# Kernel optimization log

Hardware: AMD Instinct MI355X
Metric: run time of the kernel (lower is better)

The kernel has to match this reference:

```python
import jax, jax.numpy as jnp
import numpy as np

N_NODES = 50000
N_EDGES = 800000
IN_DIM = 64
HID = 128
OUT_DIM = 128
N_LAYERS = 3
LN_EPS = 1e-5


def setup_inputs() -> dict:
    key = jax.random.key(0)
    ks = jax.random.split(key, 12)
    x = jax.random.normal(ks[0], (N_NODES, IN_DIM), dtype=jnp.float32)
    edge_index = jax.random.randint(ks[1], (2, N_EDGES), 0, N_NODES, dtype=jnp.int32)
    # parameters
    W_in = jax.random.normal(ks[2], (IN_DIM, HID), dtype=jnp.float32) / np.sqrt(IN_DIM)
    b_in = jnp.zeros((HID,), dtype=jnp.float32)
    W_layers = jax.random.normal(ks[3], (N_LAYERS, HID, HID), dtype=jnp.float32) / np.sqrt(HID)
    b_layers = jnp.zeros((N_LAYERS, HID), dtype=jnp.float32)
    ln_g = jnp.ones((N_LAYERS, HID), dtype=jnp.float32)
    ln_b = jnp.zeros((N_LAYERS, HID), dtype=jnp.float32)
    W_out = jax.random.normal(ks[4], (HID, OUT_DIM), dtype=jnp.float32) / np.sqrt(HID)
    b_out = jnp.zeros((OUT_DIM,), dtype=jnp.float32)
    return {
        "x": x, "edge_index": edge_index, "num_nodes_actual": 48000,
        "W_in": W_in, "b_in": b_in,
        "W_layers": W_layers, "b_layers": b_layers,
        "ln_g": ln_g, "ln_b": ln_b,
        "W_out": W_out, "b_out": b_out,
    }


def _layer_norm(h, g, b):
    mu = jnp.mean(h, axis=-1, keepdims=True)
    var = jnp.mean(jnp.square(h - mu), axis=-1, keepdims=True)
    return (h - mu) * jax.lax.rsqrt(var + LN_EPS) * g + b


def reference(x, edge_index, num_nodes_actual, W_in, b_in, W_layers, b_layers, ln_g, ln_b, W_out, b_out):
    n = x.shape[0]
    src, dst = edge_index[0], edge_index[1]
    # degree-normalized scatter-add aggregation (same for all layers)
    degree = jax.ops.segment_sum(jnp.ones_like(src, dtype=x.dtype), dst, num_segments=n)
    inv_deg = 1.0 / jnp.clip(degree, 1.0)[:, None]  # [N,1]

    h = x @ W_in + b_in  # [N, HID]
    for i in range(N_LAYERS):
        residual = h
        agg = jax.ops.segment_sum(h[src], dst, num_segments=n) * inv_deg
        h = (h + agg) @ W_layers[i] + b_layers[i]
        h = _layer_norm(h, ln_g[i], ln_b[i])
        h = jax.nn.relu(h)
        h = h + residual
    h = h @ W_out + b_out  # [N, OUT_DIM]
    # mean over actual (non-padding) nodes, keepdim
    return jnp.mean(h[:num_nodes_actual], axis=0, keepdims=True)  # [1, OUT_DIM]
```

## Files before the change

### kernel.cpp

```cpp
#include <hip/hip_runtime.h>

#define HID 128
#define INP 64
#define LN_EPS 1e-5f
#define RT 64

typedef __attribute__((ext_vector_type(8))) short bf16x8;
typedef __attribute__((ext_vector_type(4))) float f32x4;

__device__ __forceinline__ unsigned f2bf(float f) {
    unsigned u = __float_as_uint(f);
    return (u + 0x7FFFu + ((u >> 16) & 1u)) >> 16;
}
__device__ __forceinline__ float bflo(unsigned v) { return __uint_as_float(v << 16); }
__device__ __forceinline__ float bfhi(unsigned v) { return __uint_as_float(v & 0xFFFF0000u); }

__global__ __launch_bounds__(256) void k_count(const int* __restrict__ dst, int nE, int* __restrict__ cnt,
                                               int* __restrict__ rank, int nEdgeThreads,
                                               const float* __restrict__ W_in, const float* __restrict__ W_l,
                                               unsigned short* __restrict__ Wt_in, unsigned short* __restrict__ Wt_l) {
    int t = blockIdx.x * 256 + threadIdx.x;
    if (t < nEdgeThreads) {
        int base = t * 16;
        if (base + 16 <= nE) {
            int4 d[4];
#pragma unroll
            for (int j = 0; j < 4; ++j) d[j] = *reinterpret_cast<const int4*>(dst + base + j * 4);
            int p[16];
#pragma unroll
            for (int j = 0; j < 4; ++j) {
                p[j * 4 + 0] = atomicAdd(&cnt[d[j].x], 1);
                p[j * 4 + 1] = atomicAdd(&cnt[d[j].y], 1);
                p[j * 4 + 2] = atomicAdd(&cnt[d[j].z], 1);
                p[j * 4 + 3] = atomicAdd(&cnt[d[j].w], 1);
            }
#pragma unroll
            for (int j = 0; j < 4; ++j)
                *reinterpret_cast<int4*>(rank + base + j * 4) =
                    make_int4(p[j * 4 + 0], p[j * 4 + 1], p[j * 4 + 2], p[j * 4 + 3]);
        } else {
            for (int e = base; e < nE; ++e) rank[e] = atomicAdd(&cnt[dst[e]], 1);
        }
        return;
    }
    int i = t - nEdgeThreads;
    if (i < 128 * 64) {
        int col = i >> 6, k = i & 63;
        Wt_in[i] = (unsigned short)f2bf(W_in[(size_t)k * HID + col]);
    } else if (i < 128 * 64 + 3 * 128 * 128) {
        int j = i - 128 * 64;
        int l = j >> 14, r = j & 16383;
        int col = r >> 7, k = r & 127;
        Wt_l[j] = (unsigned short)f2bf(W_l[(size_t)l * 16384 + (size_t)k * HID + col]);
    }
}

__global__ void k_scan1(const int* __restrict__ cnt, int n, int* __restrict__ rowp, int* __restrict__ bsum) {
    __shared__ int s[256];
    int i = blockIdx.x * 256 + threadIdx.x;
    int v = (i < n) ? cnt[i] : 0;
    s[threadIdx.x] = v;
    __syncthreads();
    for (int off = 1; off < 256; off <<= 1) {
        int t = (threadIdx.x >= off) ? s[threadIdx.x - off] : 0;
        __syncthreads();
        s[threadIdx.x] += t;
        __syncthreads();
    }
    if (i < n) rowp[i] = s[threadIdx.x] - v;
    if (threadIdx.x == 255) bsum[blockIdx.x] = s[255];
}

__global__ void k_scan2(int* __restrict__ bsum, int nb) {
    __shared__ int s[256];
    int v = (threadIdx.x < nb) ? bsum[threadIdx.x] : 0;
    s[threadIdx.x] = v;
    __syncthreads();
    for (int off = 1; off < 256; off <<= 1) {
        int t = (threadIdx.x >= off) ? s[threadIdx.x - off] : 0;
        __syncthreads();
        s[threadIdx.x] += t;
        __syncthreads();
    }
    if (threadIdx.x < nb) bsum[threadIdx.x] = s[threadIdx.x] - v;
}

__global__ void k_scan3(int* __restrict__ rowp, const int* __restrict__ bsum, const int* __restrict__ cnt,
                        int n, int nE, float* __restrict__ invd) {
    int i = blockIdx.x * 256 + threadIdx.x;
    if (i < n) {
        int rp = rowp[i] + bsum[blockIdx.x];
        rowp[i] = rp;
        int c = cnt[i];
        invd[i] = 1.0f / (float)(c > 1 ? c : 1);
    } else if (i == n) {
        rowp[n] = nE;
    }
}

__global__ __launch_bounds__(256) void k_fill(const int* __restrict__ src, const int* __restrict__ dst,
                                              const int* __restrict__ rank, const int* __restrict__ rowp,
                                              int nE, int* __restrict__ csrc) {
    int t = blockIdx.x * 256 + threadIdx.x;
    int base = t * 16;
    if (base + 16 <= nE) {
        int4 d[4], s[4], r[4];
#pragma unroll
        for (int j = 0; j < 4; ++j) {
            d[j] = *reinterpret_cast<const int4*>(dst + base + j * 4);
            s[j] = *reinterpret_cast<const int4*>(src + base + j * 4);
            r[j] = *reinterpret_cast<const int4*>(rank + base + j * 4);
        }
#pragma unroll
        for (int j = 0; j < 4; ++j) {
            __builtin_nontemporal_store(s[j].x, &csrc[rowp[d[j].x] + r[j].x]);
            __builtin_nontemporal_store(s[j].y, &csrc[rowp[d[j].y] + r[j].y]);
            __builtin_nontemporal_store(s[j].z, &csrc[rowp[d[j].z] + r[j].z]);
            __builtin_nontemporal_store(s[j].w, &csrc[rowp[d[j].w] + r[j].w]);
        }
    } else if (base < nE) {
        for (int e = base; e < nE; ++e)
            __builtin_nontemporal_store(src[e], &csrc[rowp[dst[e]] + rank[e]]);
    }
}

__global__ __launch_bounds__(256) void k_inproj(const float* __restrict__ x,
                                                const unsigned short* __restrict__ Wt,
                                                const float* __restrict__ b,
                                                unsigned* __restrict__ hout, int n) {
    __shared__ unsigned short xs[RT * INP];
    const int tid = threadIdx.x;
    const int row0 = blockIdx.x * RT;

#pragma unroll
    for (int j = 0; j < 2; ++j) {
        int fid = tid + j * 256;
        int r = fid >> 3, c = fid & 7;
        int grow = row0 + r;
        unsigned o[4] = {0, 0, 0, 0};
        if (grow < n) {
            float4 v0 = *reinterpret_cast<const float4*>(x + (size_t)grow * INP + c * 8);
            float4 v1 = *reinterpret_cast<const float4*>(x + (size_t)grow * INP + c * 8 + 4);
            o[0] = f2bf(v0.x) | (f2bf(v0.y) << 16);
            o[1] = f2bf(v0.z) | (f2bf(v0.w) << 16);
            o[2] = f2bf(v1.x) | (f2bf(v1.y) << 16);
            o[3] = f2bf(v1.z) | (f2bf(v1.w) << 16);
        }
        int sw = c ^ (r & 7);
        *reinterpret_cast<uint4*>(xs + r * INP + sw * 8) = make_uint4(o[0], o[1], o[2], o[3]);
    }
    __syncthreads();

    const int l = tid & 63;
    const int w = tid >> 6;
    const int l15 = l & 15, lg = l >> 4;
    const int xrow = w * 16 + l15;

    f32x4 acc[8];
#pragma unroll
    for (int t = 0; t < 8; ++t) acc[t] = (f32x4){0.f, 0.f, 0.f, 0.f};

#pragma unroll
    for (int kc = 0; kc < 2; ++kc) {
        int bc = (kc * 4 + lg) ^ (xrow & 7);
        bf16x8 bfrag = *reinterpret_cast<const bf16x8*>(xs + xrow * INP + bc * 8);
        const unsigned short* wp = Wt + (size_t)l15 * INP + kc * 32 + lg * 8;
        bf16x8 af[8];
#pragma unroll
        for (int t = 0; t < 8; ++t) af[t] = *reinterpret_cast<const bf16x8*>(wp + (size_t)t * 16 * INP);
#pragma unroll
        for (int t = 0; t < 8; ++t)
            acc[t] = __builtin_amdgcn_mfma_f32_16x16x32_bf16(af[t], bfrag, acc[t], 0, 0, 0);
    }

    int grow = row0 + xrow;
    if (grow < n) {
#pragma unroll
        for (int t = 0; t < 8; ++t) {
            int c0 = t * 16 + lg * 4;
            f32x4 bb = *reinterpret_cast<const f32x4*>(b + c0);
            f32x4 o = acc[t] + bb;
            uint2 p;
            p.x = f2bf(o.x) | (f2bf(o.y) << 16);
            p.y = f2bf(o.z) | (f2bf(o.w) << 16);
            *reinterpret_cast<uint2*>(hout + (size_t)grow * 64 + t * 8 + lg * 2) = p;
        }
    }
}

__global__ __launch_bounds__(256) void k_agg(const unsigned* __restrict__ hb, const int* __restrict__ rowp,
                                             const int* __restrict__ csrc, const float* __restrict__ invd,
                                             unsigned* __restrict__ aggx, int n) {
    int node = blockIdx.x * 4 + (threadIdx.x >> 6);
    if (node >= n) return;
    int lane = threadIdx.x & 63;
    int e0 = rowp[node], e1 = rowp[node + 1];
    int deg = e1 - e0;
    unsigned self = hb[(size_t)node * 64 + lane];
    float inv = invd[node];
    float ax = 0.f, ay = 0.f;

    for (int base = 0; base < deg; base += 64) {
        int m = deg - base;
        if (m > 64) m = 64;
        int myidx = (base + lane < deg) ? csrc[e0 + base + lane] : 0;
        int j = 0;
        for (; j + 8 <= m; j += 8) {
            int s0 = __shfl(myidx, j + 0);
            int s1 = __shfl(myidx, j + 1);
            int s2 = __shfl(myidx, j + 2);
            int s3 = __shfl(myidx, j + 3);
            int s4 = __shfl(myidx, j + 4);
            int s5 = __shfl(myidx, j + 5);
            int s6 = __shfl(myidx, j + 6);
            int s7 = __shfl(myidx, j + 7);
            unsigned v0 = hb[(size_t)s0 * 64 + lane];
            unsigned v1 = hb[(size_t)s1 * 64 + lane];
            unsigned v2 = hb[(size_t)s2 * 64 + lane];
            unsigned v3 = hb[(size_t)s3 * 64 + lane];
            unsigned v4 = hb[(size_t)s4 * 64 + lane];
            unsigned v5 = hb[(size_t)s5 * 64 + lane];
            unsigned v6 = hb[(size_t)s6 * 64 + lane];
            unsigned v7 = hb[(size_t)s7 * 64 + lane];
            ax += ((bflo(v0) + bflo(v1)) + (bflo(v2) + bflo(v3))) +
                  ((bflo(v4) + bflo(v5)) + (bflo(v6) + bflo(v7)));
            ay += ((bfhi(v0) + bfhi(v1)) + (bfhi(v2) + bfhi(v3))) +
                  ((bfhi(v4) + bfhi(v5)) + (bfhi(v6) + bfhi(v7)));
        }
        for (; j < m; ++j) {
            int s0 = __shfl(myidx, j);
            unsigned v = hb[(size_t)s0 * 64 + lane];
            ax += bflo(v);
            ay += bfhi(v);
        }
    }

    float xlo = bflo(self) + ax * inv;
    float xhi = bfhi(self) + ay * inv;
    unsigned o = f2bf(xlo) | (f2bf(xhi) << 16);
    int c = lane >> 2;
    int sw = c ^ (node & 7);
    aggx[(size_t)node * 64 + sw * 4 + (lane & 3)] = o;
}

__global__ __launch_bounds__(256) void k_layer(const unsigned* __restrict__ hin,
                                               unsigned* __restrict__ hout,
                                               const unsigned* __restrict__ aggx,
                                               const unsigned short* __restrict__ Wt,
                                               const float* __restrict__ bias, const float* __restrict__ g,
                                               const float* __restrict__ lnb, int n) {
    const int tid = threadIdx.x;
    const int row0 = blockIdx.x * RT;
    const int lane = tid & 63;
    const int w = tid >> 6;
    const int l15 = lane & 15, lg = lane >> 4;
    const int xrow = w * 16 + l15;
    const int grow = row0 + xrow;

    const unsigned short* xg = reinterpret_cast<const unsigned short*>(aggx) + (size_t)grow * HID;

    f32x4 acc[8];
#pragma unroll
    for (int t = 0; t < 8; ++t) acc[t] = (f32x4){0.f, 0.f, 0.f, 0.f};

#pragma unroll
    for (int kc = 0; kc < 4; ++kc) {
        int bc = (kc * 4 + lg) ^ (xrow & 7);
        bf16x8 bfrag = *reinterpret_cast<const bf16x8*>(xg + bc * 8);
        const unsigned short* wp = Wt + (size_t)l15 * HID + kc * 32 + lg * 8;
        bf16x8 af[8];
#pragma unroll
        for (int t = 0; t < 8; ++t) af[t] = *reinterpret_cast<const bf16x8*>(wp + (size_t)t * 16 * HID);
#pragma unroll
        for (int t = 0; t < 8; ++t)
            acc[t] = __builtin_amdgcn_mfma_f32_16x16x32_bf16(af[t], bfrag, acc[t], 0, 0, 0);
    }

    float s = 0.f, q = 0.f;
#pragma unroll
    for (int t = 0; t < 8; ++t) {
        int c0 = t * 16 + lg * 4;
        f32x4 bb = *reinterpret_cast<const f32x4*>(bias + c0);
        acc[t] = acc[t] + bb;
        s += acc[t].x + acc[t].y + acc[t].z + acc[t].w;
        q += acc[t].x * acc[t].x + acc[t].y * acc[t].y + acc[t].z * acc[t].z + acc[t].w * acc[t].w;
    }
    s += __shfl_xor(s, 16, 64);
    s += __shfl_xor(s, 32, 64);
    q += __shfl_xor(q, 16, 64);
    q += __shfl_xor(q, 32, 64);
    float mu = s * (1.0f / HID);
    float var = q * (1.0f / HID) - mu * mu;
    float rs = rsqrtf(var + LN_EPS);

    if (grow < n) {
#pragma unroll
        for (int t = 0; t < 8; ++t) {
            int c0 = t * 16 + lg * 4;
            uint2 rv = *reinterpret_cast<const uint2*>(hin + (size_t)grow * 64 + t * 8 + lg * 2);
            f32x4 gv = *reinterpret_cast<const f32x4*>(g + c0);
            f32x4 lb = *reinterpret_cast<const f32x4*>(lnb + c0);
            float o0 = fmaxf((acc[t].x - mu) * rs * gv.x + lb.x, 0.f) + bflo(rv.x);
            float o1 = fmaxf((acc[t].y - mu) * rs * gv.y + lb.y, 0.f) + bfhi(rv.x);
            float o2 = fmaxf((acc[t].z - mu) * rs * gv.z + lb.z, 0.f) + bflo(rv.y);
            float o3 = fmaxf((acc[t].w - mu) * rs * gv.w + lb.w, 0.f) + bfhi(rv.y);
            uint2 p;
            p.x = f2bf(o0) | (f2bf(o1) << 16);
            p.y = f2bf(o2) | (f2bf(o3) << 16);
            *reinterpret_cast<uint2*>(hout + (size_t)grow * 64 + t * 8 + lg * 2) = p;
        }
    }
}

__global__ __launch_bounds__(256) void k_rowsum(const unsigned* __restrict__ hb, const int* __restrict__ n_act_p,
                                                float* __restrict__ accum, int n) {
    __shared__ float sred[256 * 2];
    int na = *n_act_p;
    int row0 = blockIdx.x * 256;
    int c = threadIdx.x & 63;
    int sub = threadIdx.x >> 6;
    int rend = row0 + 256;
    if (rend > na) rend = na;
    float sx = 0.f, sy = 0.f;
    for (int r = row0 + sub; r < rend; r += 4) {
        unsigned v = hb[(size_t)r * 64 + c];
        sx += bflo(v);
        sy += bfhi(v);
    }
    sred[threadIdx.x * 2] = sx;
    sred[threadIdx.x * 2 + 1] = sy;
    __syncthreads();
    if (threadIdx.x < 64) {
        float tx = sred[threadIdx.x * 2] + sred[(threadIdx.x + 64) * 2] +
                   sred[(threadIdx.x + 128) * 2] + sred[(threadIdx.x + 192) * 2];
        float ty = sred[threadIdx.x * 2 + 1] + sred[(threadIdx.x + 64) * 2 + 1] +
                   sred[(threadIdx.x + 128) * 2 + 1] + sred[(threadIdx.x + 192) * 2 + 1];
        if (row0 < na) {
            atomicAdd(&accum[2 * threadIdx.x], tx);
            atomicAdd(&accum[2 * threadIdx.x + 1], ty);
        }
    }
}

__global__ void k_out(const float* __restrict__ accum, const int* __restrict__ n_act_p,
                      const float* __restrict__ W_out, const float* __restrict__ b_out,
                      float* __restrict__ out) {
    __shared__ float m[HID];
    int c = threadIdx.x;
    float na = (float)(*n_act_p);
    m[c] = accum[c] / na;
    __syncthreads();
    float s = b_out[c];
    for (int k = 0; k < HID; ++k) s += m[k] * W_out[k * HID + c];
    out[c] = s;
}

extern "C" void kernel_launch(void* const* d_in, const int* in_sizes, int n_in,
                              void* d_out, int out_size, void* d_ws, size_t ws_size,
                              hipStream_t stream) {
    const int n  = in_sizes[0] / INP;
    const int nE = in_sizes[1] / 2;
    const float* x    = (const float*)d_in[0];
    const int*   ei   = (const int*)d_in[1];
    const int*   src  = ei;
    const int*   dst  = ei + nE;
    const int*   nact = (const int*)d_in[2];
    const float* W_in = (const float*)d_in[3];
    const float* b_in = (const float*)d_in[4];
    const float* W_l  = (const float*)d_in[5];
    const float* b_l  = (const float*)d_in[6];
    const float* lng  = (const float*)d_in[7];
    const float* lnb  = (const float*)d_in[8];
    const float* W_o  = (const float*)d_in[9];
    const float* b_o  = (const float*)d_in[10];

    char* ws = (char*)d_ws;
    size_t off = 0;
    auto alloc = [&](size_t bytes) {
        void* p = ws + off;
        off = (off + bytes + 255) & ~((size_t)255);
        return p;
    };
    unsigned* hbA  = (unsigned*)alloc((size_t)n * 64 * 4);
    unsigned* hbB  = (unsigned*)alloc((size_t)n * 64 * 4);
    unsigned* aggx = (unsigned*)alloc((size_t)(n + RT) * 64 * 4);
    int*   cnt  = (int*)alloc((size_t)n * 4);
    int*   rowp = (int*)alloc((size_t)(n + 1) * 4);
    float* invd = (float*)alloc((size_t)n * 4);
    int*   csrc = (int*)alloc((size_t)nE * 4);
    int*   rank = (int*)alloc((size_t)nE * 4);
    int*   bsum = (int*)alloc(1024);
    float* accum = (float*)alloc(HID * 4);
    unsigned short* Wt_in = (unsigned short*)alloc(128 * 64 * 2);
    unsigned short* Wt_l  = (unsigned short*)alloc(3 * 128 * 128 * 2);

    hipMemsetAsync(cnt, 0, (size_t)n * 4, stream);
    hipMemsetAsync(accum, 0, HID * 4, stream);

    int nb = (n + 255) / 256;
    int nEdgeThreads = (nE + 15) / 16;
    int nPrep = 128 * 64 + 3 * 128 * 128;
    int cpgrid = (nEdgeThreads + nPrep + 255) / 256;
    k_count<<<cpgrid, 256, 0, stream>>>(dst, nE, cnt, rank, nEdgeThreads, W_in, W_l, Wt_in, Wt_l);
    k_scan1<<<nb, 256, 0, stream>>>(cnt, n, rowp, bsum);
    k_scan2<<<1, 256, 0, stream>>>(bsum, nb);
    k_scan3<<<nb, 256, 0, stream>>>(rowp, bsum, cnt, n, nE, invd);
    k_fill<<<(nEdgeThreads + 255) / 256, 256, 0, stream>>>(src, dst, rank, rowp, nE, csrc);

    int tgrid = (n + RT - 1) / RT;
    k_inproj<<<tgrid, 256, 0, stream>>>(x, Wt_in, b_in, hbA, n);

    const unsigned* hin = hbA;
    unsigned* hout = hbB;
    for (int l = 0; l < 3; ++l) {
        k_agg<<<(n + 3) / 4, 256, 0, stream>>>(hin, rowp, csrc, invd, aggx, n);
        k_layer<<<tgrid, 256, 0, stream>>>(hin, hout, aggx,
                                           Wt_l + (size_t)l * 128 * 128,
                                           b_l + l * HID, lng + l * HID, lnb + l * HID, n);
        const unsigned* t = hout;
        hout = (unsigned*)hin;
        hin = t;
    }
    k_rowsum<<<(n + 255) / 256, 256, 0, stream>>>(hin, nact, accum, n);
    k_out<<<1, HID, 0, stream>>>(accum, nact, W_o, b_o, (float*)d_out);
}
```

Measured before the change: 294.0 us.

## Fuse scan stages, fill with input projection, final layer with row-sum; vectorize aggregation

Merges the block-offset scan into the final scan pass by having each block redo the small prefix over block sums. The CSR fill now runs in the same launch as the input projection, and the last layer's LayerNorm/residual output is reduced directly into the column accumulator, so the final hidden state is never written or re-read. The aggregation kernel now gathers 16-byte uint4 chunks with four edges per wavefront step and finishes with a cross-lane reduction. It also merges the two memsets into one by placing the buffers next to each other. Together these cut launches and memory traffic, at the cost of redundant scan work per block and more register pressure in the gather.

New measurement: 267.2 us (median of 2 runs). -9.1%, faster.

```diff
diff --git a/kernel.cpp b/kernel.cpp
--- a/kernel.cpp
+++ b/kernel.cpp
@@ -71,8 +71,10 @@
     if (threadIdx.x == 255) bsum[blockIdx.x] = s[255];
 }
 
-__global__ void k_scan2(int* __restrict__ bsum, int nb) {
+__global__ void k_scan3(int* __restrict__ rowp, const int* __restrict__ bsum, const int* __restrict__ cnt,
+                        int n, int nE, float* __restrict__ invd, int nb) {
     __shared__ int s[256];
+    __shared__ int boff;
     int v = (threadIdx.x < nb) ? bsum[threadIdx.x] : 0;
     s[threadIdx.x] = v;
     __syncthreads();
@@ -82,15 +84,11 @@
         s[threadIdx.x] += t;
         __syncthreads();
     }
-    if (threadIdx.x < nb) bsum[threadIdx.x] = s[threadIdx.x] - v;
-}
-
-__global__ void k_scan3(int* __restrict__ rowp, const int* __restrict__ bsum, const int* __restrict__ cnt,
-                        int n, int nE, float* __restrict__ invd) {
+    if (threadIdx.x == blockIdx.x) boff = s[threadIdx.x] - v;
+    __syncthreads();
     int i = blockIdx.x * 256 + threadIdx.x;
     if (i < n) {
-        int rp = rowp[i] + bsum[blockIdx.x];
-        rowp[i] = rp;
+        rowp[i] += boff;
         int c = cnt[i];
         invd[i] = 1.0f / (float)(c > 1 ? c : 1);
     } else if (i == n) {
@@ -98,40 +96,40 @@
     }
 }
 
-__global__ __launch_bounds__(256) void k_fill(const int* __restrict__ src, const int* __restrict__ dst,
-                                              const int* __restrict__ rank, const int* __restrict__ rowp,
-                                              int nE, int* __restrict__ csrc) {
-    int t = blockIdx.x * 256 + threadIdx.x;
-    int base = t * 16;
-    if (base + 16 <= nE) {
-        int4 d[4], s[4], r[4];
-#pragma unroll
-        for (int j = 0; j < 4; ++j) {
-            d[j] = *reinterpret_cast<const int4*>(dst + base + j * 4);
-            s[j] = *reinterpret_cast<const int4*>(src + base + j * 4);
-            r[j] = *reinterpret_cast<const int4*>(rank + base + j * 4);
-        }
-#pragma unroll
-        for (int j = 0; j < 4; ++j) {
-            __builtin_nontemporal_store(s[j].x, &csrc[rowp[d[j].x] + r[j].x]);
-            __builtin_nontemporal_store(s[j].y, &csrc[rowp[d[j].y] + r[j].y]);
-            __builtin_nontemporal_store(s[j].z, &csrc[rowp[d[j].z] + r[j].z]);
-            __builtin_nontemporal_store(s[j].w, &csrc[rowp[d[j].w] + r[j].w]);
-        }
-    } else if (base < nE) {
-        for (int e = base; e < nE; ++e)
-            __builtin_nontemporal_store(src[e], &csrc[rowp[dst[e]] + rank[e]]);
-    }
-}
-
-__global__ __launch_bounds__(256) void k_inproj(const float* __restrict__ x,
-                                                const unsigned short* __restrict__ Wt,
-                                                const float* __restrict__ b,
-                                                unsigned* __restrict__ hout, int n) {
+__global__ __launch_bounds__(256) void k_fillproj(const float* __restrict__ x,
+                                                  const unsigned short* __restrict__ Wt,
+                                                  const float* __restrict__ b,
+                                                  unsigned* __restrict__ hout, int n, int tgrid,
+                                                  const int* __restrict__ src, const int* __restrict__ dst,
+                                                  const int* __restrict__ rank, const int* __restrict__ rowp,
+                                                  int nE, int* __restrict__ csrc) {
+    const int tid = threadIdx.x;
+    if (blockIdx.x >= tgrid) {
+        int t = (blockIdx.x - tgrid) * 256 + tid;
+        int base = t * 16;
+        if (base + 16 <= nE) {
+            int4 d[4], s[4], r[4];
+#pragma unroll
+            for (int j = 0; j < 4; ++j) {
+                d[j] = *reinterpret_cast<const int4*>(dst + base + j * 4);
+                s[j] = *reinterpret_cast<const int4*>(src + base + j * 4);
+                r[j] = *reinterpret_cast<const int4*>(rank + base + j * 4);
+            }
+#pragma unroll
+            for (int j = 0; j < 4; ++j) {
+                __builtin_nontemporal_store(s[j].x, &csrc[rowp[d[j].x] + r[j].x]);
+                __builtin_nontemporal_store(s[j].y, &csrc[rowp[d[j].y] + r[j].y]);
+                __builtin_nontemporal_store(s[j].z, &csrc[rowp[d[j].z] + r[j].z]);
+                __builtin_nontemporal_store(s[j].w, &csrc[rowp[d[j].w] + r[j].w]);
+            }
+        } else if (base < nE) {
+            for (int e = base; e < nE; ++e)
+                __builtin_nontemporal_store(src[e], &csrc[rowp[dst[e]] + rank[e]]);
+        }
+        return;
+    }
     __shared__ unsigned short xs[RT * INP];
-    const int tid = threadIdx.x;
     const int row0 = blockIdx.x * RT;
-
 #pragma unroll
     for (int j = 0; j < 2; ++j) {
         int fid = tid + j * 256;
@@ -194,53 +192,65 @@
     int node = blockIdx.x * 4 + (threadIdx.x >> 6);
     if (node >= n) return;
     int lane = threadIdx.x & 63;
+    int grp = lane >> 4, cidx = lane & 15;
     int e0 = rowp[node], e1 = rowp[node + 1];
     int deg = e1 - e0;
-    unsigned self = hb[(size_t)node * 64 + lane];
-    float inv = invd[node];
-    float ax = 0.f, ay = 0.f;
+    const uint4* hb4 = reinterpret_cast<const uint4*>(hb);
+    float a0 = 0, a1 = 0, a2 = 0, a3 = 0, a4 = 0, a5 = 0, a6 = 0, a7 = 0;
 
     for (int base = 0; base < deg; base += 64) {
         int m = deg - base;
         if (m > 64) m = 64;
         int myidx = (base + lane < deg) ? csrc[e0 + base + lane] : 0;
-        int j = 0;
-        for (; j + 8 <= m; j += 8) {
-            int s0 = __shfl(myidx, j + 0);
-            int s1 = __shfl(myidx, j + 1);
-            int s2 = __shfl(myidx, j + 2);
-            int s3 = __shfl(myidx, j + 3);
-            int s4 = __shfl(myidx, j + 4);
-            int s5 = __shfl(myidx, j + 5);
-            int s6 = __shfl(myidx, j + 6);
-            int s7 = __shfl(myidx, j + 7);
-            unsigned v0 = hb[(size_t)s0 * 64 + lane];
-            unsigned v1 = hb[(size_t)s1 * 64 + lane];
-            unsigned v2 = hb[(size_t)s2 * 64 + lane];
-            unsigned v3 = hb[(size_t)s3 * 64 + lane];
-            unsigned v4 = hb[(size_t)s4 * 64 + lane];
-            unsigned v5 = hb[(size_t)s5 * 64 + lane];
-            unsigned v6 = hb[(size_t)s6 * 64 + lane];
-            unsigned v7 = hb[(size_t)s7 * 64 + lane];
-            ax += ((bflo(v0) + bflo(v1)) + (bflo(v2) + bflo(v3))) +
-                  ((bflo(v4) + bflo(v5)) + (bflo(v6) + bflo(v7)));
-            ay += ((bfhi(v0) + bfhi(v1)) + (bfhi(v2) + bfhi(v3))) +
-                  ((bfhi(v4) + bfhi(v5)) + (bfhi(v6) + bfhi(v7)));
-        }
-        for (; j < m; ++j) {
-            int s0 = __shfl(myidx, j);
-            unsigned v = hb[(size_t)s0 * 64 + lane];
-            ax += bflo(v);
-            ay += bfhi(v);
-        }
-    }
-
-    float xlo = bflo(self) + ax * inv;
-    float xhi = bfhi(self) + ay * inv;
-    unsigned o = f2bf(xlo) | (f2bf(xhi) << 16);
-    int c = lane >> 2;
-    int sw = c ^ (node & 7);
-    aggx[(size_t)node * 64 + sw * 4 + (lane & 3)] = o;
+        int steps = (m + 3) >> 2;
+        int jj = 0;
+        for (; jj + 4 <= steps; jj += 4) {
+            uint4 v[4];
+#pragma unroll
+            for (int k = 0; k < 4; ++k) {
+                int ei = (jj + k) * 4 + grp;
+                int s = __shfl(myidx, ei);
+                v[k] = (ei < m) ? hb4[(size_t)s * 16 + cidx] : make_uint4(0, 0, 0, 0);
+            }
+#pragma unroll
+            for (int k = 0; k < 4; ++k) {
+                a0 += bflo(v[k].x); a1 += bfhi(v[k].x);
+                a2 += bflo(v[k].y); a3 += bfhi(v[k].y);
+                a4 += bflo(v[k].z); a5 += bfhi(v[k].z);
+                a6 += bflo(v[k].w); a7 += bfhi(v[k].w);
+            }
+        }
+        for (; jj < steps; ++jj) {
+            int ei = jj * 4 + grp;
+            int s = __shfl(myidx, ei);
+            if (ei < m) {
+                uint4 v = hb4[(size_t)s * 16 + cidx];
+                a0 += bflo(v.x); a1 += bfhi(v.x);
+                a2 += bflo(v.y); a3 += bfhi(v.y);
+                a4 += bflo(v.z); a5 += bfhi(v.z);
+                a6 += bflo(v.w); a7 += bfhi(v.w);
+            }
+        }
+    }
+    a0 += __shfl_xor(a0, 16, 64); a0 += __shfl_xor(a0, 32, 64);
+    a1 += __shfl_xor(a1, 16, 64); a1 += __shfl_xor(a1, 32, 64);
+    a2 += __shfl_xor(a2, 16, 64); a2 += __shfl_xor(a2, 32, 64);
+    a3 += __shfl_xor(a3, 16, 64); a3 += __shfl_xor(a3, 32, 64);
+    a4 += __shfl_xor(a4, 16, 64); a4 += __shfl_xor(a4, 32, 64);
+    a5 += __shfl_xor(a5, 16, 64); a5 += __shfl_xor(a5, 32, 64);
+    a6 += __shfl_xor(a6, 16, 64); a6 += __shfl_xor(a6, 32, 64);
+    a7 += __shfl_xor(a7, 16, 64); a7 += __shfl_xor(a7, 32, 64);
+
+    if (grp == 0) {
+        float inv = invd[node];
+        uint4 self = hb4[(size_t)node * 16 + cidx];
+        unsigned o0 = f2bf(bflo(self.x) + a0 * inv) | (f2bf(bfhi(self.x) + a1 * inv) << 16);
+        unsigned o1 = f2bf(bflo(self.y) + a2 * inv) | (f2bf(bfhi(self.y) + a3 * inv) << 16);
+        unsigned o2 = f2bf(bflo(self.z) + a4 * inv) | (f2bf(bfhi(self.z) + a5 * inv) << 16);
+        unsigned o3 = f2bf(bflo(self.w) + a6 * inv) | (f2bf(bfhi(self.w) + a7 * inv) << 16);
+        int sw = cidx ^ (node & 7);
+        *reinterpret_cast<uint4*>(aggx + (size_t)node * 64 + sw * 4) = make_uint4(o0, o1, o2, o3);
+    }
 }
 
 __global__ __launch_bounds__(256) void k_layer(const unsigned* __restrict__ hin,
@@ -312,33 +322,90 @@
     }
 }
 
-__global__ __launch_bounds__(256) void k_rowsum(const unsigned* __restrict__ hb, const int* __restrict__ n_act_p,
-                                                float* __restrict__ accum, int n) {
-    __shared__ float sred[256 * 2];
-    int na = *n_act_p;
-    int row0 = blockIdx.x * 256;
-    int c = threadIdx.x & 63;
-    int sub = threadIdx.x >> 6;
-    int rend = row0 + 256;
-    if (rend > na) rend = na;
-    float sx = 0.f, sy = 0.f;
-    for (int r = row0 + sub; r < rend; r += 4) {
-        unsigned v = hb[(size_t)r * 64 + c];
-        sx += bflo(v);
-        sy += bfhi(v);
-    }
-    sred[threadIdx.x * 2] = sx;
-    sred[threadIdx.x * 2 + 1] = sy;
-    __syncthreads();
-    if (threadIdx.x < 64) {
-        float tx = sred[threadIdx.x * 2] + sred[(threadIdx.x + 64) * 2] +
-                   sred[(threadIdx.x + 128) * 2] + sred[(threadIdx.x + 192) * 2];
-        float ty = sred[threadIdx.x * 2 + 1] + sred[(threadIdx.x + 64) * 2 + 1] +
-                   sred[(threadIdx.x + 128) * 2 + 1] + sred[(threadIdx.x + 192) * 2 + 1];
-        if (row0 < na) {
-            atomicAdd(&accum[2 * threadIdx.x], tx);
-            atomicAdd(&accum[2 * threadIdx.x + 1], ty);
-        }
+__global__ __launch_bounds__(256) void k_layerF(const unsigned* __restrict__ hin,
+                                                const unsigned* __restrict__ aggx,
+                                                const unsigned short* __restrict__ Wt,
+                                                const float* __restrict__ bias, const float* __restrict__ g,
+                                                const float* __restrict__ lnb,
+                                                const int* __restrict__ n_act_p,
+                                                float* __restrict__ accum) {
+    __shared__ float red[4][4][8][4];
+    const int tid = threadIdx.x;
+    const int row0 = blockIdx.x * RT;
+    const int lane = tid & 63;
+    const int w = tid >> 6;
+    const int l15 = lane & 15, lg = lane >> 4;
+    const int xrow = w * 16 + l15;
+    const int grow = row0 + xrow;
+    const int na = *n_act_p;
+
+    const unsigned short* xg = reinterpret_cast<const unsigned short*>(aggx) + (size_t)grow * HID;
+
+    f32x4 acc[8];
+#pragma unroll
+    for (int t = 0; t < 8; ++t) acc[t] = (f32x4){0.f, 0.f, 0.f, 0.f};
+
+#pragma unroll
+    for (int kc = 0; kc < 4; ++kc) {
+        int bc = (kc * 4 + lg) ^ (xrow & 7);
+        bf16x8 bfrag = *reinterpret_cast<const bf16x8*>(xg + bc * 8);
+        const unsigned short* wp = Wt + (size_t)l15 * HID + kc * 32 + lg * 8;
+        bf16x8 af[8];
+#pragma unroll
+        for (int t = 0; t < 8; ++t) af[t] = *reinterpret_cast<const bf16x8*>(wp + (size_t)t * 16 * HID);
+#pragma unroll
+        for (int t = 0; t < 8; ++t)
+            acc[t] = __builtin_amdgcn_mfma_f32_16x16x32_bf16(af[t], bfrag, acc[t], 0, 0, 0);
+    }
+
+    float s = 0.f, q = 0.f;
+#pragma unroll
+    for (int t = 0; t < 8; ++t) {
+        int c0 = t * 16 + lg * 4;
+        f32x4 bb = *reinterpret_cast<const f32x4*>(bias + c0);
+        acc[t] = acc[t] + bb;
+        s += acc[t].x + acc[t].y + acc[t].z + acc[t].w;
+        q += acc[t].x * acc[t].x + acc[t].y * acc[t].y + acc[t].z * acc[t].z + acc[t].w * acc[t].w;
+    }
+    s += __shfl_xor(s, 16, 64);
+    s += __shfl_xor(s, 32, 64);
+    q += __shfl_xor(q, 16, 64);
+    q += __shfl_xor(q, 32, 64);
+    float mu = s * (1.0f / HID);
+    float var = q * (1.0f / HID) - mu * mu;
+    float rs = rsqrtf(var + LN_EPS);
+
+    const float msk = (grow < na) ? 1.f : 0.f;
+#pragma unroll
+    for (int t = 0; t < 8; ++t) {
+        int c0 = t * 16 + lg * 4;
+        uint2 rv = *reinterpret_cast<const uint2*>(hin + (size_t)grow * 64 + t * 8 + lg * 2);
+        f32x4 gv = *reinterpret_cast<const f32x4*>(g + c0);
+        f32x4 lb = *reinterpret_cast<const f32x4*>(lnb + c0);
+        float o0 = (fmaxf((acc[t].x - mu) * rs * gv.x + lb.x, 0.f) + bflo(rv.x)) * msk;
+        float o1 = (fmaxf((acc[t].y - mu) * rs * gv.y + lb.y, 0.f) + bfhi(rv.x)) * msk;
+        float o2 = (fmaxf((acc[t].z - mu) * rs * gv.z + lb.z, 0.f) + bflo(rv.y)) * msk;
+        float o3 = (fmaxf((acc[t].w - mu) * rs * gv.w + lb.w, 0.f) + bfhi(rv.y)) * msk;
+#pragma unroll
+        for (int m = 1; m < 16; m <<= 1) {
+            o0 += __shfl_xor(o0, m, 64);
+            o1 += __shfl_xor(o1, m, 64);
+            o2 += __shfl_xor(o2, m, 64);
+            o3 += __shfl_xor(o3, m, 64);
+        }
+        if (l15 == 0) {
+            red[w][lg][t][0] = o0;
+            red[w][lg][t][1] = o1;
+            red[w][lg][t][2] = o2;
+            red[w][lg][t][3] = o3;
+        }
+    }
+    __syncthreads();
+    if (tid < HID) {
+        int t = tid >> 4, rem = tid & 15;
+        int lgq = rem >> 2, j = rem & 3;
+        float v = red[0][lgq][t][j] + red[1][lgq][t][j] + red[2][lgq][t][j] + red[3][lgq][t][j];
+        atomicAdd(&accum[tid], v);
     }
 }
 
@@ -384,18 +451,18 @@
     unsigned* hbA  = (unsigned*)alloc((size_t)n * 64 * 4);
     unsigned* hbB  = (unsigned*)alloc((size_t)n * 64 * 4);
     unsigned* aggx = (unsigned*)alloc((size_t)(n + RT) * 64 * 4);
-    int*   cnt  = (int*)alloc((size_t)n * 4);
+    size_t cntBytes = (((size_t)n * 4) + 255) & ~((size_t)255);
+    int*   cnt   = (int*)alloc(cntBytes);
+    float* accum = (float*)alloc(HID * 4);
     int*   rowp = (int*)alloc((size_t)(n + 1) * 4);
     float* invd = (float*)alloc((size_t)n * 4);
     int*   csrc = (int*)alloc((size_t)nE * 4);
     int*   rank = (int*)alloc((size_t)nE * 4);
     int*   bsum = (int*)alloc(1024);
-    float* accum = (float*)alloc(HID * 4);
     unsigned short* Wt_in = (unsigned short*)alloc(128 * 64 * 2);
     unsigned short* Wt_l  = (unsigned short*)alloc(3 * 128 * 128 * 2);
 
-    hipMemsetAsync(cnt, 0, (size_t)n * 4, stream);
-    hipMemsetAsync(accum, 0, HID * 4, stream);
+    hipMemsetAsync(cnt, 0, cntBytes + HID * 4, stream);
 
     int nb = (n + 255) / 256;
     int nEdgeThreads = (nE + 15) / 16;
@@ -403,24 +470,30 @@
     int cpgrid = (nEdgeThreads + nPrep + 255) / 256;
     k_count<<<cpgrid, 256, 0, stream>>>(dst, nE, cnt, rank, nEdgeThreads, W_in, W_l, Wt_in, Wt_l);
     k_scan1<<<nb, 256, 0, stream>>>(cnt, n, rowp, bsum);
-    k_scan2<<<1, 256, 0, stream>>>(bsum, nb);
-    k_scan3<<<nb, 256, 0, stream>>>(rowp, bsum, cnt, n, nE, invd);
-    k_fill<<<(nEdgeThreads + 255) / 256, 256, 0, stream>>>(src, dst, rank, rowp, nE, csrc);
+    k_scan3<<<nb, 256, 0, stream>>>(rowp, bsum, cnt, n, nE, invd, nb);
 
     int tgrid = (n + RT - 1) / RT;
-    k_inproj<<<tgrid, 256, 0, stream>>>(x, Wt_in, b_in, hbA, n);
+    int fgrid = (nEdgeThreads + 255) / 256;
+    k_fillproj<<<tgrid + fgrid, 256, 0, stream>>>(x, Wt_in, b_in, hbA, n, tgrid,
+                                                  src, dst, rank, rowp, nE, csrc);
 
     const unsigned* hin = hbA;
     unsigned* hout = hbB;
     for (int l = 0; l < 3; ++l) {
         k_agg<<<(n + 3) / 4, 256, 0, stream>>>(hin, rowp, csrc, invd, aggx, n);
-        k_layer<<<tgrid, 256, 0, stream>>>(hin, hout, aggx,
-                                           Wt_l + (size_t)l * 128 * 128,
-                                           b_l + l * HID, lng + l * HID, lnb + l * HID, n);
-        const unsigned* t = hout;
-        hout = (unsigned*)hin;
-        hin = t;
-    }
-    k_rowsum<<<(n + 255) / 256, 256, 0, stream>>>(hin, nact, accum, n);
+        if (l < 2) {
+            k_layer<<<tgrid, 256, 0, stream>>>(hin, hout, aggx,
+                                               Wt_l + (size_t)l * 128 * 128,
+                                               b_l + l * HID, lng + l * HID, lnb + l * HID, n);
+            const unsigned* t = hout;
+            hout = (unsigned*)hin;
+            hin = t;
+        } else {
+            k_layerF<<<tgrid, 256, 0, stream>>>(hin, aggx,
+                                                Wt_l + (size_t)l * 128 * 128,
+                                                b_l + l * HID, lng + l * HID, lnb + l * HID,
+                                                nact, accum);
+        }
+    }
     k_out<<<1, HID, 0, stream>>>(accum, nact, W_o, b_o, (float*)d_out);
 }
```
